# Kernel optimization log

Hardware: AMD Instinct MI355X
Metric: run time of the kernel (lower is better)

The kernel has to match this reference:

```python
import jax, jax.numpy as jnp
import numpy as np

NUM_HEADS = 4
EPS = 1e-5

def _proj(x, W, b):
    # 1x1x1 Conv3d == channel-wise linear: x [B,C,H,W,D], W [Cout,Cin], b [Cout]
    return jnp.einsum('oc,bchwd->bohwd', W, x) + b[None, :, None, None, None]

def setup_inputs() -> dict:
    key = jax.random.key(0)
    ks = jax.random.split(key, 12)
    B, C, H, W, D = 2, 128, 16, 16, 16
    s = 1.0 / np.sqrt(C)
    inp = {
        'query_features': jax.random.normal(ks[0], (B, C, H, W, D), jnp.float32),
        'key_value_features': jax.random.normal(ks[1], (B, C, H, W, D), jnp.float32),
        'Wq': jax.random.normal(ks[2], (C, C), jnp.float32) * s,
        'bq': jax.random.normal(ks[3], (C,), jnp.float32) * 0.01,
        'Wk': jax.random.normal(ks[4], (C, C), jnp.float32) * s,
        'bk': jax.random.normal(ks[5], (C,), jnp.float32) * 0.01,
        'Wv': jax.random.normal(ks[6], (C, C), jnp.float32) * s,
        'bv': jax.random.normal(ks[7], (C,), jnp.float32) * 0.01,
        'Wo': jax.random.normal(ks[8], (C, C), jnp.float32) * s,
        'bo': jax.random.normal(ks[9], (C,), jnp.float32) * 0.01,
    }
    return inp

def reference(query_features, key_value_features, Wq, bq, Wk, bk, Wv, bv, Wo, bo):
    B, C, H, W, D = query_features.shape
    hd = C // NUM_HEADS  # head_dim
    N = H * W * D
    Q = _proj(query_features, Wq, bq).reshape(B, NUM_HEADS, hd, N)
    K = _proj(key_value_features, Wk, bk).reshape(B, NUM_HEADS, hd, N)
    V = _proj(key_value_features, Wv, bv).reshape(B, NUM_HEADS, hd, N)
    scale = hd ** -0.5
    attn = jnp.einsum('bhdn,bhdm->bhnm', Q, K) * scale  # [B,h,N,N]
    attn = jax.nn.softmax(attn, axis=-1)
    out = jnp.einsum('bhnm,bhdm->bhdn', attn, V).reshape(B, C, H, W, D)
    out = _proj(out, Wo, bo)
    res = query_features + out
    # InstanceNorm3d (affine=False): normalize over spatial dims per (B,C)
    mu = jnp.mean(res, axis=(2, 3, 4), keepdims=True)
    var = jnp.var(res, axis=(2, 3, 4), keepdims=True)
    return (res - mu) * jax.lax.rsqrt(var + EPS)
```

## Files before the change

### kernel.cpp

```cpp
#include <hip/hip_runtime.h>
#include <hip/hip_bf16.h>

typedef unsigned short u16;
typedef unsigned int u32;
typedef __bf16 bf16_t;
typedef bf16_t bf16x8 __attribute__((ext_vector_type(8)));
typedef float f32x4 __attribute__((ext_vector_type(4)));

#define NTOT 4096
#define CCH 128
#define QSCL 0.25503486703f

__device__ __forceinline__ float bf2f(u16 x) {
    return __uint_as_float(((u32)x) << 16);
}
__device__ __forceinline__ u32 pkbf(float a, float b) {
    __hip_bfloat162 h = __float22bfloat162_rn(make_float2(a, b));
    u32 r; __builtin_memcpy(&r, &h, 4); return r;
}
__device__ __forceinline__ u16 f2bf(float a) {
    return (u16)(pkbf(a, a) & 0xffffu);
}
__device__ __forceinline__ bf16x8 ldv(const u16* p) {
    uint2 lo = *(const uint2*)(p);
    uint2 hi = *(const uint2*)(p + 16);
    uint4 u = {lo.x, lo.y, hi.x, hi.y};
    bf16x8 r; __builtin_memcpy(&r, &u, 16); return r;
}

__global__ __launch_bounds__(256, 4) void proj_kernel(
    const float* __restrict__ xq, const float* __restrict__ xkv,
    const float* __restrict__ Wq, const float* __restrict__ bq,
    const float* __restrict__ Wk, const float* __restrict__ bk_,
    const float* __restrict__ Wv, const float* __restrict__ bv_,
    u16* __restrict__ Qt, u16* __restrict__ Kt, u16* __restrict__ Vn)
{
    const int nt = blockIdx.x, p = blockIdx.y, b = blockIdx.z;
    const float* X    = (p == 0) ? xq : xkv;
    const float* Wf   = (p == 0) ? Wq : (p == 1) ? Wk : Wv;
    const float* bias = (p == 0) ? bq : (p == 1) ? bk_ : bv_;
    const float s = (p == 0) ? QSCL : 1.0f;
    const int n0 = nt * 64;
    const int tid = threadIdx.x;

    __shared__ u16 Xt[64 * 128];
    __shared__ u16 Wl[128 * 136];

    #pragma unroll
    for (int k = 0; k < 4; ++k) {
        int n = tid & 63;
        int c = (tid >> 6) + k * 4;
        float f[8];
        #pragma unroll
        for (int j = 0; j < 8; ++j)
            f[j] = X[((size_t)(b * CCH) + 8 * c + j) * NTOT + n0 + n];
        uint4 vv = {pkbf(f[0], f[1]), pkbf(f[2], f[3]), pkbf(f[4], f[5]), pkbf(f[6], f[7])};
        *(uint4*)(Xt + n * 128 + ((c ^ (n & 7)) * 8)) = vv;
    }
    #pragma unroll
    for (int k = 0; k < 8; ++k) {
        int id = tid + k * 256;
        int row = id >> 4;
        int off = (id & 15) * 8;
        const float* wsrc = Wf + row * 128 + off;
        float4 wa = *(const float4*)(wsrc);
        float4 wc = *(const float4*)(wsrc + 4);
        uint4 vv = {pkbf(wa.x * s, wa.y * s), pkbf(wa.z * s, wa.w * s),
                    pkbf(wc.x * s, wc.y * s), pkbf(wc.z * s, wc.w * s)};
        *(uint4*)(Wl + row * 136 + off) = vv;
    }
    __syncthreads();

    const int wave = tid >> 6, lane = tid & 63;
    const int quad = lane >> 4, l16 = lane & 15;
    f32x4 acc[8];
    #pragma unroll
    for (int cf = 0; cf < 8; ++cf) acc[cf] = (f32x4){0.f, 0.f, 0.f, 0.f};

    #pragma unroll
    for (int kk = 0; kk < 4; ++kk) {
        bf16x8 bx = *(const bf16x8*)(Xt + (wave * 16 + l16) * 128 +
                                     (((kk * 4 + quad) ^ (l16 & 7)) * 8));
        #pragma unroll
        for (int cf = 0; cf < 8; ++cf) {
            bf16x8 aw = *(const bf16x8*)(Wl + (cf * 16 + l16) * 136 + kk * 32 + quad * 8);
            acc[cf] = __builtin_amdgcn_mfma_f32_16x16x32_bf16(aw, bx, acc[cf], 0, 0, 0);
        }
    }

    const int n = n0 + wave * 16 + l16;
    #pragma unroll
    for (int cf = 0; cf < 8; ++cf) {
        float4 b4 = *(const float4*)(bias + cf * 16 + quad * 4);
        float v0 = acc[cf][0] + b4.x * s;
        float v1 = acc[cf][1] + b4.y * s;
        float v2 = acc[cf][2] + b4.z * s;
        float v3 = acc[cf][3] + b4.w * s;
        if (p < 2) {
            const int h = cf >> 1;
            const int d0 = (cf & 1) * 16 + quad * 4;
            u16* dst = (p == 0 ? Qt : Kt) + ((size_t)(b * 4 + h) * NTOT + n) * 32 + d0;
            uint2 vv = {pkbf(v0, v1), pkbf(v2, v3)};
            *(uint2*)dst = vv;
        } else {
            int c = cf * 16 + quad * 4;
            u16* dst = Vn + (size_t)(b * CCH + c) * NTOT + n;
            dst[0 * NTOT] = f2bf(v0); dst[1 * NTOT] = f2bf(v1);
            dst[2 * NTOT] = f2bf(v2); dst[3 * NTOT] = f2bf(v3);
        }
    }
}

__global__ __launch_bounds__(256, 2) void flash_attn_kernel(
    const u16* __restrict__ Qt, const u16* __restrict__ Kt,
    const u16* __restrict__ Vn, u16* __restrict__ pO, float* __restrict__ pL)
{
    const int bh = blockIdx.z, kc = blockIdx.y;
    const int wave = threadIdx.x >> 6, lane = threadIdx.x & 63;
    const int q = lane >> 4, l16 = lane & 15;
    const int q0w = blockIdx.x * 256 + wave * 64;

    const u16* Qbh = Qt + (size_t)bh * NTOT * 32;
    const u16* Kbh = Kt + (size_t)bh * NTOT * 32;
    const u16* Vg  = Vn + ((size_t)((bh >> 2) * CCH + (bh & 3) * 32)) * NTOT;

    const int kbase = kc * 1024;

    bf16x8 bq[4];
    #pragma unroll
    for (int g = 0; g < 4; ++g)
        bq[g] = *(const bf16x8*)(Qbh + (size_t)(q0w + g * 16 + l16) * 32 + q * 8);

    const u16* kp  = Kbh + (size_t)(kbase + l16) * 32 + q * 8;
    const u16* vp0 = Vg + (size_t)l16 * NTOT + kbase + q * 4;
    const u16* vp1 = vp0 + (size_t)16 * NTOT;

    f32x4 o[4][2];
    #pragma unroll
    for (int g = 0; g < 4; ++g) {
        o[g][0] = (f32x4){0,0,0,0};
        o[g][1] = (f32x4){0,0,0,0};
    }
    const f32x4 zero = {0,0,0,0};
    float lp[4] = {0.f, 0.f, 0.f, 0.f};

    bf16x8 ak[4], av[4];
    #pragma unroll
    for (int t = 0; t < 4; ++t)
        ak[t] = *(const bf16x8*)(kp + (size_t)(t * 16) * 32);
    #pragma unroll
    for (int r = 0; r < 4; ++r)
        av[r] = ldv(((r & 1) ? vp1 : vp0) + (r >> 1) * 32);

    for (int it = 0; it < 16; ++it) {
        bf16x8 nak[4], nav[4];
        if (it < 15) {
            const int m1 = (it + 1) * 64;
            #pragma unroll
            for (int t = 0; t < 4; ++t)
                nak[t] = *(const bf16x8*)(kp + (size_t)(m1 + t * 16) * 32);
            #pragma unroll
            for (int r = 0; r < 4; ++r)
                nav[r] = ldv(((r & 1) ? vp1 : vp0) + m1 + (r >> 1) * 32);
        }
        f32x4 s[4][4];
        #pragma unroll
        for (int t = 0; t < 4; ++t) {
            #pragma unroll
            for (int g = 0; g < 4; ++g)
                s[g][t] = __builtin_amdgcn_mfma_f32_16x16x32_bf16(ak[t], bq[g], zero, 0, 0, 0);
        }
        #pragma unroll
        for (int g = 0; g < 4; ++g) {
            float e[4][4];
            #pragma unroll
            for (int t = 0; t < 4; ++t) {
                e[t][0] = __builtin_amdgcn_exp2f(s[g][t][0]);
                e[t][1] = __builtin_amdgcn_exp2f(s[g][t][1]);
                e[t][2] = __builtin_amdgcn_exp2f(s[g][t][2]);
                e[t][3] = __builtin_amdgcn_exp2f(s[g][t][3]);
                lp[g] += (e[t][0] + e[t][1]) + (e[t][2] + e[t][3]);
            }
            uint4 u0 = {pkbf(e[0][0], e[0][1]), pkbf(e[0][2], e[0][3]),
                        pkbf(e[1][0], e[1][1]), pkbf(e[1][2], e[1][3])};
            uint4 u1 = {pkbf(e[2][0], e[2][1]), pkbf(e[2][2], e[2][3]),
                        pkbf(e[3][0], e[3][1]), pkbf(e[3][2], e[3][3])};
            bf16x8 pb0, pb1;
            __builtin_memcpy(&pb0, &u0, 16);
            __builtin_memcpy(&pb1, &u1, 16);
            o[g][0] = __builtin_amdgcn_mfma_f32_16x16x32_bf16(av[0], pb0, o[g][0], 0, 0, 0);
            o[g][1] = __builtin_amdgcn_mfma_f32_16x16x32_bf16(av[1], pb0, o[g][1], 0, 0, 0);
            o[g][0] = __builtin_amdgcn_mfma_f32_16x16x32_bf16(av[2], pb1, o[g][0], 0, 0, 0);
            o[g][1] = __builtin_amdgcn_mfma_f32_16x16x32_bf16(av[3], pb1, o[g][1], 0, 0, 0);
        }
        if (it < 15) {
            #pragma unroll
            for (int t = 0; t < 4; ++t) ak[t] = nak[t];
            #pragma unroll
            for (int r = 0; r < 4; ++r) av[r] = nav[r];
        }
    }

    #pragma unroll
    for (int g = 0; g < 4; ++g) {
        lp[g] += __shfl_xor(lp[g], 16);
        lp[g] += __shfl_xor(lp[g], 32);
        const size_t ob = ((size_t)(kc * 8 + bh) * NTOT + q0w + g * 16 + l16) * 32 + q * 4;
        uint2 w0 = {pkbf(o[g][0][0], o[g][0][1]), pkbf(o[g][0][2], o[g][0][3])};
        uint2 w1 = {pkbf(o[g][1][0], o[g][1][1]), pkbf(o[g][1][2], o[g][1][3])};
        *(uint2*)(pO + ob)      = w0;
        *(uint2*)(pO + ob + 16) = w1;
        if (q == 0)
            pL[(size_t)(kc * 8 + bh) * NTOT + q0w + g * 16 + l16] = lp[g];
    }
}

__global__ __launch_bounds__(256, 4) void outproj_kernel(
    const float* __restrict__ xq,
    const u16* __restrict__ pO, const float* __restrict__ pL,
    const float* __restrict__ Wo, const float* __restrict__ bo,
    float* __restrict__ res, float* __restrict__ partS, float* __restrict__ partQ)
{
    const int nt = blockIdx.x, ct = blockIdx.y, b = blockIdx.z;
    const int n0 = nt * 64;
    const int tid = threadIdx.x;

    __shared__ u16 Xt[64 * 128];
    __shared__ u16 Wl[64 * 136];

    #pragma unroll
    for (int k = 0; k < 4; ++k) {
        int cid = tid + k * 256;
        int n = cid >> 4;
        int ch = cid & 15;
        int bh = b * 4 + (ch >> 2);
        int d0 = (ch & 3) * 8;
        float l = 0.f;
        float v[8];
        #pragma unroll
        for (int j = 0; j < 8; ++j) v[j] = 0.f;
        #pragma unroll
        for (int kcc = 0; kcc < 4; ++kcc) {
            const size_t nrow = (size_t)(kcc * 8 + bh) * NTOT + n0 + n;
            l += pL[nrow];
            uint4 u = *(const uint4*)(pO + nrow * 32 + d0);
            const u32 uu[4] = {u.x, u.y, u.z, u.w};
            #pragma unroll
            for (int j = 0; j < 4; ++j) {
                v[2 * j]     += bf2f((u16)(uu[j] & 0xffffu));
                v[2 * j + 1] += bf2f((u16)(uu[j] >> 16));
            }
        }
        const float inv = 1.0f / l;
        uint4 vv = {pkbf(v[0] * inv, v[1] * inv), pkbf(v[2] * inv, v[3] * inv),
                    pkbf(v[4] * inv, v[5] * inv), pkbf(v[6] * inv, v[7] * inv)};
        *(uint4*)(Xt + n * 128 + ((ch ^ (n & 7)) * 8)) = vv;
    }
    #pragma unroll
    for (int k = 0; k < 4; ++k) {
        int id = tid + k * 256;
        int row = id >> 4;
        int off = (id & 15) * 8;
        const float* wsrc = Wo + (size_t)(ct * 64 + row) * 128 + off;
        float4 wa = *(const float4*)(wsrc);
        float4 wc = *(const float4*)(wsrc + 4);
        uint4 vv = {pkbf(wa.x, wa.y), pkbf(wa.z, wa.w),
                    pkbf(wc.x, wc.y), pkbf(wc.z, wc.w)};
        *(uint4*)(Wl + row * 136 + off) = vv;
    }
    __syncthreads();

    const int wave = tid >> 6, lane = tid & 63;
    const int quad = lane >> 4, l16 = lane & 15;
    f32x4 acc[4];
    #pragma unroll
    for (int cf = 0; cf < 4; ++cf) acc[cf] = (f32x4){0.f, 0.f, 0.f, 0.f};

    #pragma unroll
    for (int kk = 0; kk < 4; ++kk) {
        bf16x8 bx = *(const bf16x8*)(Xt + (wave * 16 + l16) * 128 +
                                     (((kk * 4 + quad) ^ (l16 & 7)) * 8));
        #pragma unroll
        for (int cf = 0; cf < 4; ++cf) {
            bf16x8 aw = *(const bf16x8*)(Wl + (cf * 16 + l16) * 136 + kk * 32 + quad * 8);
            acc[cf] = __builtin_amdgcn_mfma_f32_16x16x32_bf16(aw, bx, acc[cf], 0, 0, 0);
        }
    }

    const int n = n0 + wave * 16 + l16;
    const int tile = nt * 4 + wave;
    #pragma unroll
    for (int cf = 0; cf < 4; ++cf) {
        float4 b4 = *(const float4*)(bo + ct * 64 + cf * 16 + quad * 4);
        const float bb[4] = {b4.x, b4.y, b4.z, b4.w};
        float sv[4], qv[4];
        #pragma unroll
        for (int r = 0; r < 4; ++r) {
            int c = ct * 64 + cf * 16 + quad * 4 + r;
            float v = acc[cf][r] + bb[r] + xq[(size_t)(b * CCH + c) * NTOT + n];
            res[(size_t)(b * CCH + c) * NTOT + n] = v;
            sv[r] = v;
            qv[r] = v * v;
        }
        #pragma unroll
        for (int off = 1; off < 16; off <<= 1) {
            #pragma unroll
            for (int r = 0; r < 4; ++r) {
                sv[r] += __shfl_xor(sv[r], off);
                qv[r] += __shfl_xor(qv[r], off);
            }
        }
        if (l16 == 0) {
            #pragma unroll
            for (int r = 0; r < 4; ++r) {
                int c = ct * 64 + cf * 16 + quad * 4 + r;
                partS[(size_t)(b * CCH + c) * 256 + tile] = sv[r];
                partQ[(size_t)(b * CCH + c) * 256 + tile] = qv[r];
            }
        }
    }
}

__global__ __launch_bounds__(256) void norm_kernel(
    const float* __restrict__ res, const float* __restrict__ partS,
    const float* __restrict__ partQ, float* __restrict__ out)
{
    const int c = blockIdx.x, b = blockIdx.y;
    const int tid = threadIdx.x;
    const size_t row = (size_t)(b * CCH + c);
    __shared__ float rs[4], rq[4];
    float s = partS[row * 256 + tid];
    float q = partQ[row * 256 + tid];
    #pragma unroll
    for (int off = 1; off < 64; off <<= 1) {
        s += __shfl_xor(s, off);
        q += __shfl_xor(q, off);
    }
    const int wv = tid >> 6, ln = tid & 63;
    if (ln == 0) { rs[wv] = s; rq[wv] = q; }
    __syncthreads();
    float ts = rs[0] + rs[1] + rs[2] + rs[3];
    float tq = rq[0] + rq[1] + rq[2] + rq[3];
    float mu  = ts * (1.0f / 4096.0f);
    float var = tq * (1.0f / 4096.0f) - mu * mu;
    float inv = rsqrtf(var + 1e-5f);
    const size_t base = row * NTOT;
    #pragma unroll
    for (int j = 0; j < 4; ++j) {
        int n = tid * 4 + j * 1024;
        float4 v = *(const float4*)(res + base + n);
        float4 o;
        o.x = (v.x - mu) * inv; o.y = (v.y - mu) * inv;
        o.z = (v.z - mu) * inv; o.w = (v.w - mu) * inv;
        *(float4*)(out + base + n) = o;
    }
}

extern "C" void kernel_launch(void* const* d_in, const int* in_sizes, int n_in,
                              void* d_out, int out_size, void* d_ws, size_t ws_size,
                              hipStream_t stream)
{
    const float* xq  = (const float*)d_in[0];
    const float* xkv = (const float*)d_in[1];
    const float* Wq  = (const float*)d_in[2];
    const float* bq  = (const float*)d_in[3];
    const float* Wk  = (const float*)d_in[4];
    const float* bk  = (const float*)d_in[5];
    const float* Wv  = (const float*)d_in[6];
    const float* bv  = (const float*)d_in[7];
    const float* Wo  = (const float*)d_in[8];
    const float* bo  = (const float*)d_in[9];
    float* out = (float*)d_out;

    char* ws = (char*)d_ws;
    const size_t MB = (size_t)1 << 20;
    u16* Qt = (u16*)(ws + 0 * MB);
    u16* Kt = (u16*)(ws + 2 * MB);
    u16* Vn = (u16*)(ws + 4 * MB);
    u16* pO = (u16*)(ws + 6 * MB);
    float* pL = (float*)(ws + 14 * MB);
    float* res   = (float*)(ws + 16 * MB);
    float* partS = (float*)(ws + 20 * MB);
    float* partQ = (float*)(ws + 20 * MB + 262144);

    proj_kernel<<<dim3(64, 3, 2), 256, 0, stream>>>(xq, xkv, Wq, bq, Wk, bk, Wv, bv, Qt, Kt, Vn);
    flash_attn_kernel<<<dim3(16, 4, 8), 256, 0, stream>>>(Qt, Kt, Vn, pO, pL);
    outproj_kernel<<<dim3(64, 2, 2), 256, 0, stream>>>(xq, pO, pL, Wo, bo, res, partS, partQ);
    norm_kernel<<<dim3(128, 2), 256, 0, stream>>>(res, partS, partQ, out);
}
```

Measured before the change: 131.7 us.

## Stage K/V chunks in shared memory and split keys into eight chunks

The flash attention kernel now has the block cooperatively load its 512-key chunk of K and V into LDS, pre-swizzled into MFMA fragment layout, and then read fragments from LDS. Before, each wave loaded K/V fragments directly from global memory. The key dimension is split into 8 chunks instead of 4, which doubles the grid. The out-projection kernel then reduces 8 partial outputs, and the workspace offsets are enlarged to fit. This aims to remove redundant global loads across the four waves and raise parallelism. In exchange it adds 64KB of LDS per block, which may limit occupancy, plus more partial-sum traffic.

```diff
diff --git a/kernel.cpp b/kernel.cpp
--- a/kernel.cpp
+++ b/kernel.cpp
@@ -20,12 +20,6 @@
 }
 __device__ __forceinline__ u16 f2bf(float a) {
     return (u16)(pkbf(a, a) & 0xffffu);
-}
-__device__ __forceinline__ bf16x8 ldv(const u16* p) {
-    uint2 lo = *(const uint2*)(p);
-    uint2 hi = *(const uint2*)(p + 16);
-    uint4 u = {lo.x, lo.y, hi.x, hi.y};
-    bf16x8 r; __builtin_memcpy(&r, &u, 16); return r;
 }
 
 __global__ __launch_bounds__(256, 4) void proj_kernel(
@@ -124,16 +118,35 @@
     const u16* Kbh = Kt + (size_t)bh * NTOT * 32;
     const u16* Vg  = Vn + ((size_t)((bh >> 2) * CCH + (bh & 3) * 32)) * NTOT;
 
-    const int kbase = kc * 1024;
+    __shared__ u16 Ksh[8 * 2048];
+    __shared__ u16 Vsh[8 * 2048];
+
+    const int kbase = kc * 512;
 
     bf16x8 bq[4];
     #pragma unroll
     for (int g = 0; g < 4; ++g)
         bq[g] = *(const bf16x8*)(Qbh + (size_t)(q0w + g * 16 + l16) * 32 + q * 8);
 
-    const u16* kp  = Kbh + (size_t)(kbase + l16) * 32 + q * 8;
-    const u16* vp0 = Vg + (size_t)l16 * NTOT + kbase + q * 4;
-    const u16* vp1 = vp0 + (size_t)16 * NTOT;
+    {
+        const size_t kst = (size_t)(kbase + wave * 16 + l16) * 32 + q * 8;
+        const size_t vst = (size_t)((wave & 1) * 16 + l16) * NTOT + kbase +
+                           (wave >> 1) * 32 + q * 8;
+        const int kds = wave * 512 + lane * 8;
+        const int vds = wave * 512 + (q & 1) * 256 + l16 * 8 + (q >> 1) * 4;
+        #pragma unroll
+        for (int m = 0; m < 8; ++m) {
+            uint4 kr = *(const uint4*)(Kbh + kst + m * 2048);
+            uint4 vr = *(const uint4*)(Vg + vst + m * 64);
+            *(uint4*)(&Ksh[m * 2048 + kds]) = kr;
+            uint2 va = {kr.x, kr.y};
+            va.x = vr.x; va.y = vr.y;
+            uint2 vb = {vr.z, vr.w};
+            *(uint2*)(&Vsh[m * 2048 + vds])       = va;
+            *(uint2*)(&Vsh[m * 2048 + vds + 128]) = vb;
+        }
+    }
+    __syncthreads();
 
     f32x4 o[4][2];
     #pragma unroll
@@ -144,24 +157,23 @@
     const f32x4 zero = {0,0,0,0};
     float lp[4] = {0.f, 0.f, 0.f, 0.f};
 
+    const int frd = lane * 8;
     bf16x8 ak[4], av[4];
     #pragma unroll
-    for (int t = 0; t < 4; ++t)
-        ak[t] = *(const bf16x8*)(kp + (size_t)(t * 16) * 32);
-    #pragma unroll
-    for (int r = 0; r < 4; ++r)
-        av[r] = ldv(((r & 1) ? vp1 : vp0) + (r >> 1) * 32);
-
-    for (int it = 0; it < 16; ++it) {
+    for (int t = 0; t < 4; ++t) {
+        ak[t] = *(const bf16x8*)(&Ksh[t * 512 + frd]);
+        av[t] = *(const bf16x8*)(&Vsh[t * 512 + frd]);
+    }
+
+    for (int m = 0; m < 8; ++m) {
         bf16x8 nak[4], nav[4];
-        if (it < 15) {
-            const int m1 = (it + 1) * 64;
-            #pragma unroll
-            for (int t = 0; t < 4; ++t)
-                nak[t] = *(const bf16x8*)(kp + (size_t)(m1 + t * 16) * 32);
-            #pragma unroll
-            for (int r = 0; r < 4; ++r)
-                nav[r] = ldv(((r & 1) ? vp1 : vp0) + m1 + (r >> 1) * 32);
+        if (m < 7) {
+            const int nb = (m + 1) * 2048;
+            #pragma unroll
+            for (int t = 0; t < 4; ++t) {
+                nak[t] = *(const bf16x8*)(&Ksh[nb + t * 512 + frd]);
+                nav[t] = *(const bf16x8*)(&Vsh[nb + t * 512 + frd]);
+            }
         }
         f32x4 s[4][4];
         #pragma unroll
@@ -193,11 +205,9 @@
             o[g][0] = __builtin_amdgcn_mfma_f32_16x16x32_bf16(av[2], pb1, o[g][0], 0, 0, 0);
             o[g][1] = __builtin_amdgcn_mfma_f32_16x16x32_bf16(av[3], pb1, o[g][1], 0, 0, 0);
         }
-        if (it < 15) {
-            #pragma unroll
-            for (int t = 0; t < 4; ++t) ak[t] = nak[t];
-            #pragma unroll
-            for (int r = 0; r < 4; ++r) av[r] = nav[r];
+        if (m < 7) {
+            #pragma unroll
+            for (int t = 0; t < 4; ++t) { ak[t] = nak[t]; av[t] = nav[t]; }
         }
     }
 
@@ -240,7 +250,7 @@
         #pragma unroll
         for (int j = 0; j < 8; ++j) v[j] = 0.f;
         #pragma unroll
-        for (int kcc = 0; kcc < 4; ++kcc) {
+        for (int kcc = 0; kcc < 8; ++kcc) {
             const size_t nrow = (size_t)(kcc * 8 + bh) * NTOT + n0 + n;
             l += pL[nrow];
             uint4 u = *(const uint4*)(pO + nrow * 32 + d0);
@@ -378,13 +388,13 @@
     u16* Kt = (u16*)(ws + 2 * MB);
     u16* Vn = (u16*)(ws + 4 * MB);
     u16* pO = (u16*)(ws + 6 * MB);
-    float* pL = (float*)(ws + 14 * MB);
-    float* res   = (float*)(ws + 16 * MB);
-    float* partS = (float*)(ws + 20 * MB);
-    float* partQ = (float*)(ws + 20 * MB + 262144);
+    float* pL = (float*)(ws + 22 * MB);
+    float* res   = (float*)(ws + 23 * MB);
+    float* partS = (float*)(ws + 27 * MB);
+    float* partQ = (float*)(ws + 27 * MB + 262144);
 
     proj_kernel<<<dim3(64, 3, 2), 256, 0, stream>>>(xq, xkv, Wq, bq, Wk, bk, Wv, bv, Qt, Kt, Vn);
-    flash_attn_kernel<<<dim3(16, 4, 8), 256, 0, stream>>>(Qt, Kt, Vn, pO, pL);
+    flash_attn_kernel<<<dim3(16, 8, 8), 256, 0, stream>>>(Qt, Kt, Vn, pO, pL);
     outproj_kernel<<<dim3(64, 2, 2), 256, 0, stream>>>(xq, pO, pL, Wo, bo, res, partS, partQ);
     norm_kernel<<<dim3(128, 2), 256, 0, stream>>>(res, partS, partQ, out);
 }
```

After: 121.0 us. -8.1%, faster.
